# Optimization experiments

Hardware: AMD Instinct MI355X
Metric: run time of the kernel (lower is better)

## Reference

```python
import jax, jax.numpy as jnp
import numpy as np

E = 20    # number of residue types (rc.restypes)
NB = 2    # num_blocks per AngleHead
NA = 7    # num_angles
C_S = 384
C_H = 128
BS, L = 8, 2048


def setup_inputs() -> dict:
    key = jax.random.key(0)
    ks = jax.random.split(key, 16)
    sc = 0.02
    return {
        "s": jax.random.normal(ks[0], (BS, L, C_S), dtype=jnp.float32),
        "s_init": jax.random.normal(ks[1], (BS, L, C_S), dtype=jnp.float32),
        "aatype": jax.random.randint(ks[2], (BS, L), 0, E, dtype=jnp.int32),
        # stacked per-residue-type AngleHead params
        "Win": jax.random.normal(ks[3], (E, C_S, C_H), dtype=jnp.float32) * sc,
        "b_in": jax.random.normal(ks[4], (E, C_H), dtype=jnp.float32) * sc,
        "Winit": jax.random.normal(ks[5], (E, C_S, C_H), dtype=jnp.float32) * sc,
        "b_init2": jax.random.normal(ks[6], (E, C_H), dtype=jnp.float32) * sc,
        "Wb1": jax.random.normal(ks[7], (E, NB, C_H, C_H), dtype=jnp.float32) * sc,
        "bb1": jax.random.normal(ks[8], (E, NB, C_H), dtype=jnp.float32) * sc,
        "Wb2": jax.random.normal(ks[9], (E, NB, C_H, C_H), dtype=jnp.float32) * sc,
        "bb2": jax.random.normal(ks[10], (E, NB, C_H), dtype=jnp.float32) * sc,
        "Wout": jax.random.normal(ks[11], (E, C_H, NA * 2), dtype=jnp.float32) * sc,
        "b_out": jax.random.normal(ks[12], (E, NA * 2), dtype=jnp.float32) * sc,
    }


def reference(s, s_init, aatype, Win, b_in, Winit, b_init2, Wb1, bb1, Wb2, bb2, Wout, b_out):
    relu = jax.nn.relu
    bs, seq_len, c_s = s.shape
    N = bs * seq_len
    sf = s.reshape(N, c_s)          # [N, c_s]
    si = s_init.reshape(N, c_s)     # [N, c_s]

    # Dense dispatch: run every token through all E per-type heads, then
    # combine with the one-hot routing mask (math identical to the torch
    # gather/scatter loop over residue types).
    h = jnp.einsum('nd,edh->neh', relu(sf), Win) + b_in            # [N,E,H]
    h = h + jnp.einsum('nd,edh->neh', relu(si), Winit) + b_init2   # [N,E,H]

    for b in range(NB):  # ResidualBlock1d: s + W2 @ relu(W1 @ relu(s))
        a = jnp.einsum('neh,ehk->nek', relu(h), Wb1[:, b]) + bb1[:, b]
        a = jnp.einsum('nek,ekh->neh', relu(a), Wb2[:, b]) + bb2[:, b]
        h = h + a

    out = jnp.einsum('neh,eho->neo', relu(h), Wout) + b_out        # [N,E,2*NA]
    sel = jax.nn.one_hot(aatype.reshape(N), E, dtype=out.dtype)    # [N,E]
    ang = jnp.einsum('neo,ne->no', out, sel).reshape(bs, seq_len, NA, 2)

    # F.normalize(dim=-1): x / max(||x||, eps)
    nrm = jnp.maximum(jnp.linalg.norm(ang, axis=-1, keepdims=True), 1e-12)
    return ang / nrm
```

## Files before the change

### kernel.cpp

```cpp
#include <hip/hip_runtime.h>
#include <math.h>

#define E_TYPES 20
#define NBLK 2
#define NANG 7
#define CS 384
#define CH 128
#define N_TOK (8 * 2048)
#define TOK 32
#define TPB 256
#define KC 128
#define MAX_TILES (N_TOK / TOK + E_TYPES)
#define NPREP 64

#define HIST_OFF 0
#define CNT_OFF 1536
#define POFF_OFF 1600
#define PERM_OFF 2048

#define WT1_OFF (256 * 1024)
#define WT1_SZ  (20 * 8 * 24 * 2048)
#define WTR_OFF (WT1_OFF + WT1_SZ)

typedef __attribute__((ext_vector_type(8))) short bfrag;
typedef __attribute__((ext_vector_type(4))) float f32x4;

__device__ __forceinline__ void split_bf16(float x, unsigned short& h, unsigned short& l) {
    unsigned int u = __float_as_uint(x);
    unsigned int hb = (u + 0x7FFFu + ((u >> 16) & 1u)) & 0xFFFF0000u;
    h = (unsigned short)(hb >> 16);
    float r = x - __uint_as_float(hb);
    unsigned int v = __float_as_uint(r);
    l = (unsigned short)((v + 0x7FFFu + ((v >> 16) & 1u)) >> 16);
}

__global__ void prep1(const float* __restrict__ Win, const float* __restrict__ Winit,
                      const float* __restrict__ Wb1, const float* __restrict__ Wb2,
                      const int* __restrict__ aatype, int* __restrict__ wsI,
                      unsigned short* __restrict__ wt) {
    __shared__ int lh[E_TYPES];
    int bid = blockIdx.x;
    int t = threadIdx.x;
    if (bid >= 1600) {
        int b2 = bid - 1600;
        if (t < E_TYPES) lh[t] = 0;
        __syncthreads();
        int idx = b2 * 256 + t;
        if (idx < N_TOK) atomicAdd(&lh[aatype[idx]], 1);
        __syncthreads();
        if (t < E_TYPES) wsI[HIST_OFF + b2 * E_TYPES + t] = lh[t];
        return;
    }
    int gid = bid * 256 + t;
    unsigned short h[8], l[8];
    if (gid < 245760) {
        int lane = gid & 63;
        int bi = gid >> 6;
        int kb = bi % 24;
        int r = bi / 24;
        int nt = r & 7, e = r >> 3;
        int n = nt * 16 + (lane & 15);
        int k0 = kb * 32 + (lane >> 4) * 8;
        #pragma unroll
        for (int j = 0; j < 8; j++) {
            int k = k0 + j;
            float x = (k < CS) ? Win[((size_t)e * CS + k) * CH + n]
                               : Winit[((size_t)e * CS + (k - CS)) * CH + n];
            split_bf16(x, h[j], l[j]);
        }
        unsigned short* dst = wt + (WT1_OFF / 2) + (size_t)bi * 1024 + lane * 8;
        *(bfrag*)dst = *(bfrag*)h;
        *(bfrag*)(dst + 512) = *(bfrag*)l;
    } else {
        gid -= 245760;
        int lane = gid & 63;
        int bi = gid >> 6;
        int kb = bi & 3;
        int nt = (bi >> 2) & 7;
        int m4 = (bi >> 5) & 3;
        int e = bi >> 7;
        int b = m4 >> 1;
        const float* W = (m4 & 1) ? Wb2 : Wb1;
        int n = nt * 16 + (lane & 15);
        int k0 = kb * 32 + (lane >> 4) * 8;
        #pragma unroll
        for (int j = 0; j < 8; j++) {
            int k = k0 + j;
            float x = W[(((size_t)e * NBLK + b) * CH + k) * CH + n];
            split_bf16(x, h[j], l[j]);
        }
        unsigned short* dst = wt + (WTR_OFF / 2) + (size_t)bi * 1024 + lane * 8;
        *(bfrag*)dst = *(bfrag*)h;
        *(bfrag*)(dst + 512) = *(bfrag*)l;
    }
}

__global__ void scatter_k(const int* __restrict__ aatype, int* ws) {
    __shared__ int lhist[NPREP * E_TYPES];
    __shared__ int counts[E_TYPES], poff[E_TYPES + 1], mybase[E_TYPES], lcur[E_TYPES];
    int t = threadIdx.x;
    int bid = blockIdx.x;
    for (int idx = t; idx < NPREP * E_TYPES; idx += TPB)
        lhist[idx] = ws[HIST_OFF + idx];
    if (t < E_TYPES) lcur[t] = 0;
    __syncthreads();
    if (t < E_TYPES) {
        int tot = 0, pre = 0;
        for (int b = 0; b < NPREP; b++) {
            int v = lhist[b * E_TYPES + t];
            tot += v;
            if (b < bid) pre += v;
        }
        counts[t] = tot;
        mybase[t] = pre;
    }
    __syncthreads();
    if (t == 0) {
        int off = 0;
        for (int e = 0; e < E_TYPES; e++) {
            poff[e] = off;
            off += (counts[e] + TOK - 1) & ~(TOK - 1);
        }
        poff[E_TYPES] = off;
    }
    __syncthreads();
    if (t < E_TYPES) mybase[t] += poff[t];
    __syncthreads();
    int idx = bid * blockDim.x + t;
    if (idx < N_TOK) {
        int e = aatype[idx];
        int r = atomicAdd(&lcur[e], 1);
        ws[PERM_OFF + mybase[e] + r] = idx;
    }
    if (bid == 0) {
        if (t < E_TYPES) ws[CNT_OFF + t] = counts[t];
        if (t == 0)
            for (int e = 0; e <= E_TYPES; e++) ws[POFF_OFF + e] = poff[e];
    }
}

#define MFMA(a, b, c) __builtin_amdgcn_mfma_f32_16x16x32_bf16((a), (b), (c), 0, 0, 0)

__global__ __launch_bounds__(TPB)
void angle_main(const float* __restrict__ s, const float* __restrict__ si,
                const float* __restrict__ b_in, const float* __restrict__ b_init2,
                const float* __restrict__ bb1, const float* __restrict__ bb2,
                const float* __restrict__ Wout, const float* __restrict__ b_out,
                const int* __restrict__ wsI, const unsigned short* __restrict__ wt,
                float* __restrict__ out)
{
    __shared__ unsigned short Ah[TOK][136];
    __shared__ unsigned short Al[TOK][136];
    __shared__ float Hf[TOK][132];
    __shared__ float Of[TOK][16];
    __shared__ int ptok[TOK];

    int pos = blockIdx.x * TOK;
    if (pos >= wsI[POFF_OFF + E_TYPES]) return;
    int e = 0;
    while (e < E_TYPES - 1 && pos >= wsI[POFF_OFF + e + 1]) e++;
    int n = wsI[CNT_OFF + e] - (pos - wsI[POFF_OFF + e]);
    if (n > TOK) n = TOK;

    int t = threadIdx.x;
    if (t < TOK) ptok[t] = wsI[PERM_OFF + pos + ((t < n) ? t : 0)];

    int w = t >> 6, lane = t & 63;
    int lane15 = lane & 15, quad = lane >> 4;
    int nc[2] = { (2 * w) * 16 + lane15, (2 * w + 1) * 16 + lane15 };

    const bfrag* wt1 = (const bfrag*)((const char*)wt + WT1_OFF);
    const bfrag* wtr = (const bfrag*)((const char*)wt + WTR_OFF);

    f32x4 acc[2][2];
    {
        float bv0 = b_in[e * CH + nc[0]] + b_init2[e * CH + nc[0]];
        float bv1 = b_in[e * CH + nc[1]] + b_init2[e * CH + nc[1]];
        #pragma unroll
        for (int mt = 0; mt < 2; mt++) {
            acc[mt][0] = (f32x4){bv0, bv0, bv0, bv0};
            acc[mt][1] = (f32x4){bv1, bv1, bv1, bv1};
        }
    }

    __syncthreads();

    int srow = t >> 3;
    int scol = (t & 7) * 16;
    for (int c = 0; c < 6; c++) {
        const float* src = (c < 3) ? s : si;
        int kb0 = (c < 3 ? c : c - 3) * KC;
        {
            const float4* rp = (const float4*)(src + (size_t)ptok[srow] * CS + kb0 + scol);
            #pragma unroll
            for (int q = 0; q < 4; q++) {
                float4 v = rp[q];
                ushort4 hv, lv;
                split_bf16(fmaxf(v.x, 0.f), hv.x, lv.x);
                split_bf16(fmaxf(v.y, 0.f), hv.y, lv.y);
                split_bf16(fmaxf(v.z, 0.f), hv.z, lv.z);
                split_bf16(fmaxf(v.w, 0.f), hv.w, lv.w);
                *(ushort4*)&Ah[srow][scol + 4 * q] = hv;
                *(ushort4*)&Al[srow][scol + 4 * q] = lv;
            }
        }
        __syncthreads();
        #pragma unroll
        for (int ks = 0; ks < 4; ks++) {
            int kb = c * 4 + ks;
            int kl = ks * 32 + quad * 8;
            bfrag ah0 = *(const bfrag*)&Ah[lane15][kl];
            bfrag ah1 = *(const bfrag*)&Ah[16 + lane15][kl];
            bfrag al0 = *(const bfrag*)&Al[lane15][kl];
            bfrag al1 = *(const bfrag*)&Al[16 + lane15][kl];
            size_t b0 = ((size_t)(e * 8 + 2 * w) * 24 + kb) * 128;
            size_t b1 = ((size_t)(e * 8 + 2 * w + 1) * 24 + kb) * 128;
            bfrag bh0 = wt1[b0 + lane],      bl0 = wt1[b0 + 64 + lane];
            bfrag bh1 = wt1[b1 + lane],      bl1 = wt1[b1 + 64 + lane];
            acc[0][0] = MFMA(ah0, bh0, acc[0][0]);
            acc[0][0] = MFMA(ah0, bl0, acc[0][0]);
            acc[0][0] = MFMA(al0, bh0, acc[0][0]);
            acc[0][1] = MFMA(ah0, bh1, acc[0][1]);
            acc[0][1] = MFMA(ah0, bl1, acc[0][1]);
            acc[0][1] = MFMA(al0, bh1, acc[0][1]);
            acc[1][0] = MFMA(ah1, bh0, acc[1][0]);
            acc[1][0] = MFMA(ah1, bl0, acc[1][0]);
            acc[1][0] = MFMA(al1, bh0, acc[1][0]);
            acc[1][1] = MFMA(ah1, bh1, acc[1][1]);
            acc[1][1] = MFMA(ah1, bl1, acc[1][1]);
            acc[1][1] = MFMA(al1, bh1, acc[1][1]);
        }
        __syncthreads();
    }

    for (int b = 0; b < NBLK; b++) {
        #pragma unroll
        for (int mt = 0; mt < 2; mt++)
            #pragma unroll
            for (int nl = 0; nl < 2; nl++) {
                f32x4 v = acc[mt][nl];
                #pragma unroll
                for (int r = 0; r < 4; r++) {
                    int m = mt * 16 + quad * 4 + r;
                    unsigned short hh, ll;
                    split_bf16(fmaxf(v[r], 0.f), hh, ll);
                    Ah[m][nc[nl]] = hh;
                    Al[m][nc[nl]] = ll;
                }
            }
        __syncthreads();

        f32x4 a2[2][2];
        {
            float bv0 = bb1[(e * NBLK + b) * CH + nc[0]];
            float bv1 = bb1[(e * NBLK + b) * CH + nc[1]];
            #pragma unroll
            for (int mt = 0; mt < 2; mt++) {
                a2[mt][0] = (f32x4){bv0, bv0, bv0, bv0};
                a2[mt][1] = (f32x4){bv1, bv1, bv1, bv1};
            }
        }
        #pragma unroll
        for (int ks = 0; ks < 4; ks++) {
            int kl = ks * 32 + quad * 8;
            bfrag ah0 = *(const bfrag*)&Ah[lane15][kl];
            bfrag ah1 = *(const bfrag*)&Ah[16 + lane15][kl];
            bfrag al0 = *(const bfrag*)&Al[lane15][kl];
            bfrag al1 = *(const bfrag*)&Al[16 + lane15][kl];
            size_t b0 = (((size_t)(e * 4 + 2 * b) * 8 + 2 * w) * 4 + ks) * 128;
            size_t b1 = (((size_t)(e * 4 + 2 * b) * 8 + 2 * w + 1) * 4 + ks) * 128;
            bfrag bh0 = wtr[b0 + lane], bl0 = wtr[b0 + 64 + lane];
            bfrag bh1 = wtr[b1 + lane], bl1 = wtr[b1 + 64 + lane];
            a2[0][0] = MFMA(ah0, bh0, a2[0][0]);
            a2[0][0] = MFMA(ah0, bl0, a2[0][0]);
            a2[0][0] = MFMA(al0, bh0, a2[0][0]);
            a2[0][1] = MFMA(ah0, bh1, a2[0][1]);
            a2[0][1] = MFMA(ah0, bl1, a2[0][1]);
            a2[0][1] = MFMA(al0, bh1, a2[0][1]);
            a2[1][0] = MFMA(ah1, bh0, a2[1][0]);
            a2[1][0] = MFMA(ah1, bl0, a2[1][0]);
            a2[1][0] = MFMA(al1, bh0, a2[1][0]);
            a2[1][1] = MFMA(ah1, bh1, a2[1][1]);
            a2[1][1] = MFMA(ah1, bl1, a2[1][1]);
            a2[1][1] = MFMA(al1, bh1, a2[1][1]);
        }
        __syncthreads();

        #pragma unroll
        for (int mt = 0; mt < 2; mt++)
            #pragma unroll
            for (int nl = 0; nl < 2; nl++) {
                f32x4 v = a2[mt][nl];
                #pragma unroll
                for (int r = 0; r < 4; r++) {
                    int m = mt * 16 + quad * 4 + r;
                    unsigned short hh, ll;
                    split_bf16(fmaxf(v[r], 0.f), hh, ll);
                    Ah[m][nc[nl]] = hh;
                    Al[m][nc[nl]] = ll;
                }
            }
        __syncthreads();

        f32x4 a3[2][2];
        {
            float bv0 = bb2[(e * NBLK + b) * CH + nc[0]];
            float bv1 = bb2[(e * NBLK + b) * CH + nc[1]];
            #pragma unroll
            for (int mt = 0; mt < 2; mt++) {
                a3[mt][0] = (f32x4){bv0, bv0, bv0, bv0};
                a3[mt][1] = (f32x4){bv1, bv1, bv1, bv1};
            }
        }
        #pragma unroll
        for (int ks = 0; ks < 4; ks++) {
            int kl = ks * 32 + quad * 8;
            bfrag ah0 = *(const bfrag*)&Ah[lane15][kl];
            bfrag ah1 = *(const bfrag*)&Ah[16 + lane15][kl];
            bfrag al0 = *(const bfrag*)&Al[lane15][kl];
            bfrag al1 = *(const bfrag*)&Al[16 + lane15][kl];
            size_t b0 = (((size_t)(e * 4 + 2 * b + 1) * 8 + 2 * w) * 4 + ks) * 128;
            size_t b1 = (((size_t)(e * 4 + 2 * b + 1) * 8 + 2 * w + 1) * 4 + ks) * 128;
            bfrag bh0 = wtr[b0 + lane], bl0 = wtr[b0 + 64 + lane];
            bfrag bh1 = wtr[b1 + lane], bl1 = wtr[b1 + 64 + lane];
            a3[0][0] = MFMA(ah0, bh0, a3[0][0]);
            a3[0][0] = MFMA(ah0, bl0, a3[0][0]);
            a3[0][0] = MFMA(al0, bh0, a3[0][0]);
            a3[0][1] = MFMA(ah0, bh1, a3[0][1]);
            a3[0][1] = MFMA(ah0, bl1, a3[0][1]);
            a3[0][1] = MFMA(al0, bh1, a3[0][1]);
            a3[1][0] = MFMA(ah1, bh0, a3[1][0]);
            a3[1][0] = MFMA(ah1, bl0, a3[1][0]);
            a3[1][0] = MFMA(al1, bh0, a3[1][0]);
            a3[1][1] = MFMA(ah1, bh1, a3[1][1]);
            a3[1][1] = MFMA(ah1, bl1, a3[1][1]);
            a3[1][1] = MFMA(al1, bh1, a3[1][1]);
        }
        #pragma unroll
        for (int mt = 0; mt < 2; mt++)
            #pragma unroll
            for (int nl = 0; nl < 2; nl++)
                acc[mt][nl] += a3[mt][nl];
        __syncthreads();
    }

    #pragma unroll
    for (int mt = 0; mt < 2; mt++)
        #pragma unroll
        for (int nl = 0; nl < 2; nl++) {
            f32x4 v = acc[mt][nl];
            #pragma unroll
            for (int r = 0; r < 4; r++)
                Hf[mt * 16 + quad * 4 + r][nc[nl]] = fmaxf(v[r], 0.f);
        }
    __syncthreads();

    const float* WoutE = Wout + (size_t)e * CH * (NANG * 2);
    const float* boutE = b_out + (size_t)e * (NANG * 2);
    for (int idx = t; idx < n * (NANG * 2); idx += TPB) {
        int i = idx / (NANG * 2);
        int o = idx % (NANG * 2);
        float v = boutE[o];
        #pragma unroll 4
        for (int k = 0; k < CH; k++)
            v = fmaf(Hf[i][k], WoutE[(size_t)k * (NANG * 2) + o], v);
        Of[i][o] = v;
    }
    __syncthreads();

    for (int idx = t; idx < n * NANG; idx += TPB) {
        int i = idx / NANG;
        int a = idx % NANG;
        float x = Of[i][2 * a];
        float y = Of[i][2 * a + 1];
        float nr = fmaxf(sqrtf(x * x + y * y), 1e-12f);
        size_t base = (size_t)ptok[i] * (NANG * 2) + 2 * a;
        out[base]     = x / nr;
        out[base + 1] = y / nr;
    }
}

extern "C" void kernel_launch(void* const* d_in, const int* in_sizes, int n_in,
                              void* d_out, int out_size, void* d_ws, size_t ws_size,
                              hipStream_t stream) {
    const float* s       = (const float*)d_in[0];
    const float* s_init  = (const float*)d_in[1];
    const int*   aatype  = (const int*)d_in[2];
    const float* Win     = (const float*)d_in[3];
    const float* b_in    = (const float*)d_in[4];
    const float* Winit   = (const float*)d_in[5];
    const float* b_init2 = (const float*)d_in[6];
    const float* Wb1     = (const float*)d_in[7];
    const float* bb1     = (const float*)d_in[8];
    const float* Wb2     = (const float*)d_in[9];
    const float* bb2     = (const float*)d_in[10];
    const float* Wout    = (const float*)d_in[11];
    const float* b_out   = (const float*)d_in[12];
    int* wsI = (int*)d_ws;
    unsigned short* wt = (unsigned short*)d_ws;
    float* out = (float*)d_out;

    hipLaunchKernelGGL(prep1, dim3(1664), dim3(256), 0, stream,
                       Win, Winit, Wb1, Wb2, aatype, wsI, wt);
    hipLaunchKernelGGL(scatter_k, dim3(NPREP), dim3(TPB), 0, stream, aatype, wsI);
    hipLaunchKernelGGL(angle_main, dim3(MAX_TILES), dim3(TPB), 0, stream,
                       s, s_init, b_in, b_init2, bb1, bb2, Wout, b_out,
                       wsI, wt, out);
}
```

Before: 160.0 us.

## Use 512-thread blocks in main kernel with one column tile per wave and prefetch

```diff
diff --git a/kernel.cpp b/kernel.cpp
--- a/kernel.cpp
+++ b/kernel.cpp
@@ -9,6 +9,7 @@
 #define N_TOK (8 * 2048)
 #define TOK 32
 #define TPB 256
+#define TPB_MAIN 512
 #define KC 128
 #define MAX_TILES (N_TOK / TOK + E_TYPES)
 #define NPREP 64
@@ -141,7 +142,7 @@
 
 #define MFMA(a, b, c) __builtin_amdgcn_mfma_f32_16x16x32_bf16((a), (b), (c), 0, 0, 0)
 
-__global__ __launch_bounds__(TPB)
+__global__ __launch_bounds__(TPB_MAIN)
 void angle_main(const float* __restrict__ s, const float* __restrict__ si,
                 const float* __restrict__ b_in, const float* __restrict__ b_init2,
                 const float* __restrict__ bb1, const float* __restrict__ bb2,
@@ -167,44 +168,43 @@
 
     int w = t >> 6, lane = t & 63;
     int lane15 = lane & 15, quad = lane >> 4;
-    int nc[2] = { (2 * w) * 16 + lane15, (2 * w + 1) * 16 + lane15 };
+    int nc = w * 16 + lane15;
 
     const bfrag* wt1 = (const bfrag*)((const char*)wt + WT1_OFF);
     const bfrag* wtr = (const bfrag*)((const char*)wt + WTR_OFF);
 
-    f32x4 acc[2][2];
+    f32x4 acc[2];
     {
-        float bv0 = b_in[e * CH + nc[0]] + b_init2[e * CH + nc[0]];
-        float bv1 = b_in[e * CH + nc[1]] + b_init2[e * CH + nc[1]];
-        #pragma unroll
-        for (int mt = 0; mt < 2; mt++) {
-            acc[mt][0] = (f32x4){bv0, bv0, bv0, bv0};
-            acc[mt][1] = (f32x4){bv1, bv1, bv1, bv1};
-        }
-    }
-
-    __syncthreads();
-
-    int srow = t >> 3;
-    int scol = (t & 7) * 16;
+        float bv = b_in[e * CH + nc] + b_init2[e * CH + nc];
+        acc[0] = (f32x4){bv, bv, bv, bv};
+        acc[1] = acc[0];
+    }
+
+    __syncthreads();
+
+    int srow = t >> 4;
+    int scol = (t & 15) * 8;
+    size_t rowoff = (size_t)ptok[srow] * CS + scol;
+    float4 p0 = *(const float4*)(s + rowoff);
+    float4 p1 = *(const float4*)(s + rowoff + 4);
+
     for (int c = 0; c < 6; c++) {
-        const float* src = (c < 3) ? s : si;
-        int kb0 = (c < 3 ? c : c - 3) * KC;
         {
-            const float4* rp = (const float4*)(src + (size_t)ptok[srow] * CS + kb0 + scol);
+            float xv[8] = {p0.x, p0.y, p0.z, p0.w, p1.x, p1.y, p1.z, p1.w};
+            unsigned short h8[8], l8[8];
             #pragma unroll
-            for (int q = 0; q < 4; q++) {
-                float4 v = rp[q];
-                ushort4 hv, lv;
-                split_bf16(fmaxf(v.x, 0.f), hv.x, lv.x);
-                split_bf16(fmaxf(v.y, 0.f), hv.y, lv.y);
-                split_bf16(fmaxf(v.z, 0.f), hv.z, lv.z);
-                split_bf16(fmaxf(v.w, 0.f), hv.w, lv.w);
-                *(ushort4*)&Ah[srow][scol + 4 * q] = hv;
-                *(ushort4*)&Al[srow][scol + 4 * q] = lv;
-            }
-        }
-        __syncthreads();
+            for (int j = 0; j < 8; j++)
+                split_bf16(fmaxf(xv[j], 0.f), h8[j], l8[j]);
+            *(bfrag*)&Ah[srow][scol] = *(bfrag*)h8;
+            *(bfrag*)&Al[srow][scol] = *(bfrag*)l8;
+        }
+        __syncthreads();
+        if (c < 5) {
+            const float* src = (c + 1 < 3) ? s : si;
+            int kb0 = ((c + 1 < 3) ? (c + 1) : (c - 2)) * KC;
+            p0 = *(const float4*)(src + rowoff + kb0);
+            p1 = *(const float4*)(src + rowoff + kb0 + 4);
+        }
         #pragma unroll
         for (int ks = 0; ks < 4; ks++) {
             int kb = c * 4 + ks;
@@ -213,52 +213,39 @@
             bfrag ah1 = *(const bfrag*)&Ah[16 + lane15][kl];
             bfrag al0 = *(const bfrag*)&Al[lane15][kl];
             bfrag al1 = *(const bfrag*)&Al[16 + lane15][kl];
-            size_t b0 = ((size_t)(e * 8 + 2 * w) * 24 + kb) * 128;
-            size_t b1 = ((size_t)(e * 8 + 2 * w + 1) * 24 + kb) * 128;
-            bfrag bh0 = wt1[b0 + lane],      bl0 = wt1[b0 + 64 + lane];
-            bfrag bh1 = wt1[b1 + lane],      bl1 = wt1[b1 + 64 + lane];
-            acc[0][0] = MFMA(ah0, bh0, acc[0][0]);
-            acc[0][0] = MFMA(ah0, bl0, acc[0][0]);
-            acc[0][0] = MFMA(al0, bh0, acc[0][0]);
-            acc[0][1] = MFMA(ah0, bh1, acc[0][1]);
-            acc[0][1] = MFMA(ah0, bl1, acc[0][1]);
-            acc[0][1] = MFMA(al0, bh1, acc[0][1]);
-            acc[1][0] = MFMA(ah1, bh0, acc[1][0]);
-            acc[1][0] = MFMA(ah1, bl0, acc[1][0]);
-            acc[1][0] = MFMA(al1, bh0, acc[1][0]);
-            acc[1][1] = MFMA(ah1, bh1, acc[1][1]);
-            acc[1][1] = MFMA(ah1, bl1, acc[1][1]);
-            acc[1][1] = MFMA(al1, bh1, acc[1][1]);
+            size_t b0 = ((size_t)(e * 8 + w) * 24 + kb) * 128;
+            bfrag bh = wt1[b0 + lane];
+            bfrag bl = wt1[b0 + 64 + lane];
+            acc[0] = MFMA(ah0, bh, acc[0]);
+            acc[0] = MFMA(ah0, bl, acc[0]);
+            acc[0] = MFMA(al0, bh, acc[0]);
+            acc[1] = MFMA(ah1, bh, acc[1]);
+            acc[1] = MFMA(ah1, bl, acc[1]);
+            acc[1] = MFMA(al1, bh, acc[1]);
         }
         __syncthreads();
     }
 
     for (int b = 0; b < NBLK; b++) {
         #pragma unroll
-        for (int mt = 0; mt < 2; mt++)
+        for (int mt = 0; mt < 2; mt++) {
+            f32x4 v = acc[mt];
             #pragma unroll
-            for (int nl = 0; nl < 2; nl++) {
-                f32x4 v = acc[mt][nl];
-                #pragma unroll
-                for (int r = 0; r < 4; r++) {
-                    int m = mt * 16 + quad * 4 + r;
-                    unsigned short hh, ll;
-                    split_bf16(fmaxf(v[r], 0.f), hh, ll);
-                    Ah[m][nc[nl]] = hh;
-                    Al[m][nc[nl]] = ll;
-                }
+            for (int r = 0; r < 4; r++) {
+                int m = mt * 16 + quad * 4 + r;
+                unsigned short hh, ll;
+                split_bf16(fmaxf(v[r], 0.f), hh, ll);
+                Ah[m][nc] = hh;
+                Al[m][nc] = ll;
             }
-        __syncthreads();
-
-        f32x4 a2[2][2];
+        }
+        __syncthreads();
+
+        f32x4 a2[2];
         {
-            float bv0 = bb1[(e * NBLK + b) * CH + nc[0]];
-            float bv1 = bb1[(e * NBLK + b) * CH + nc[1]];
-            #pragma unroll
-            for (int mt = 0; mt < 2; mt++) {
-                a2[mt][0] = (f32x4){bv0, bv0, bv0, bv0};
-                a2[mt][1] = (f32x4){bv1, bv1, bv1, bv1};
-            }
+            float bv = bb1[(e * NBLK + b) * CH + nc];
+            a2[0] = (f32x4){bv, bv, bv, bv};
+            a2[1] = a2[0];
         }
         #pragma unroll
         for (int ks = 0; ks < 4; ks++) {
@@ -267,50 +254,36 @@
             bfrag ah1 = *(const bfrag*)&Ah[16 + lane15][kl];
             bfrag al0 = *(const bfrag*)&Al[lane15][kl];
             bfrag al1 = *(const bfrag*)&Al[16 + lane15][kl];
-            size_t b0 = (((size_t)(e * 4 + 2 * b) * 8 + 2 * w) * 4 + ks) * 128;
-            size_t b1 = (((size_t)(e * 4 + 2 * b) * 8 + 2 * w + 1) * 4 + ks) * 128;
-            bfrag bh0 = wtr[b0 + lane], bl0 = wtr[b0 + 64 + lane];
-            bfrag bh1 = wtr[b1 + lane], bl1 = wtr[b1 + 64 + lane];
-            a2[0][0] = MFMA(ah0, bh0, a2[0][0]);
-            a2[0][0] = MFMA(ah0, bl0, a2[0][0]);
-            a2[0][0] = MFMA(al0, bh0, a2[0][0]);
-            a2[0][1] = MFMA(ah0, bh1, a2[0][1]);
-            a2[0][1] = MFMA(ah0, bl1, a2[0][1]);
-            a2[0][1] = MFMA(al0, bh1, a2[0][1]);
-            a2[1][0] = MFMA(ah1, bh0, a2[1][0]);
-            a2[1][0] = MFMA(ah1, bl0, a2[1][0]);
-            a2[1][0] = MFMA(al1, bh0, a2[1][0]);
-            a2[1][1] = MFMA(ah1, bh1, a2[1][1]);
-            a2[1][1] = MFMA(ah1, bl1, a2[1][1]);
-            a2[1][1] = MFMA(al1, bh1, a2[1][1]);
-        }
-        __syncthreads();
-
-        #pragma unroll
-        for (int mt = 0; mt < 2; mt++)
+            size_t b0 = (((size_t)(e * 4 + 2 * b) * 8 + w) * 4 + ks) * 128;
+            bfrag bh = wtr[b0 + lane], bl = wtr[b0 + 64 + lane];
+            a2[0] = MFMA(ah0, bh, a2[0]);
+            a2[0] = MFMA(ah0, bl, a2[0]);
+            a2[0] = MFMA(al0, bh, a2[0]);
+            a2[1] = MFMA(ah1, bh, a2[1]);
+            a2[1] = MFMA(ah1, bl, a2[1]);
+            a2[1] = MFMA(al1, bh, a2[1]);
+        }
+        __syncthreads();
+
+        #pragma unroll
+        for (int mt = 0; mt < 2; mt++) {
+            f32x4 v = a2[mt];
             #pragma unroll
-            for (int nl = 0; nl < 2; nl++) {
-                f32x4 v = a2[mt][nl];
-                #pragma unroll
-                for (int r = 0; r < 4; r++) {
-                    int m = mt * 16 + quad * 4 + r;
-                    unsigned short hh, ll;
-                    split_bf16(fmaxf(v[r], 0.f), hh, ll);
-                    Ah[m][nc[nl]] = hh;
-                    Al[m][nc[nl]] = ll;
-                }
+            for (int r = 0; r < 4; r++) {
+                int m = mt * 16 + quad * 4 + r;
+                unsigned short hh, ll;
+                split_bf16(fmaxf(v[r], 0.f), hh, ll);
+                Ah[m][nc] = hh;
+                Al[m][nc] = ll;
             }
-        __syncthreads();
-
-        f32x4 a3[2][2];
+        }
+        __syncthreads();
+
+        f32x4 a3[2];
         {
-            float bv0 = bb2[(e * NBLK + b) * CH + nc[0]];
-            float bv1 = bb2[(e * NBLK + b) * CH + nc[1]];
-            #pragma unroll
-            for (int mt = 0; mt < 2; mt++) {
-                a3[mt][0] = (f32x4){bv0, bv0, bv0, bv0};
-                a3[mt][1] = (f32x4){bv1, bv1, bv1, bv1};
-            }
+            float bv = bb2[(e * NBLK + b) * CH + nc];
+            a3[0] = (f32x4){bv, bv, bv, bv};
+            a3[1] = a3[0];
         }
         #pragma unroll
         for (int ks = 0; ks < 4; ks++) {
@@ -319,58 +292,49 @@
             bfrag ah1 = *(const bfrag*)&Ah[16 + lane15][kl];
             bfrag al0 = *(const bfrag*)&Al[lane15][kl];
             bfrag al1 = *(const bfrag*)&Al[16 + lane15][kl];
-            size_t b0 = (((size_t)(e * 4 + 2 * b + 1) * 8 + 2 * w) * 4 + ks) * 128;
-            size_t b1 = (((size_t)(e * 4 + 2 * b + 1) * 8 + 2 * w + 1) * 4 + ks) * 128;
-            bfrag bh0 = wtr[b0 + lane], bl0 = wtr[b0 + 64 + lane];
-            bfrag bh1 = wtr[b1 + lane], bl1 = wtr[b1 + 64 + lane];
-            a3[0][0] = MFMA(ah0, bh0, a3[0][0]);
-            a3[0][0] = MFMA(ah0, bl0, a3[0][0]);
-            a3[0][0] = MFMA(al0, bh0, a3[0][0]);
-            a3[0][1] = MFMA(ah0, bh1, a3[0][1]);
-            a3[0][1] = MFMA(ah0, bl1, a3[0][1]);
-            a3[0][1] = MFMA(al0, bh1, a3[0][1]);
-            a3[1][0] = MFMA(ah1, bh0, a3[1][0]);
-            a3[1][0] = MFMA(ah1, bl0, a3[1][0]);
-            a3[1][0] = MFMA(al1, bh0, a3[1][0]);
-            a3[1][1] = MFMA(ah1, bh1, a3[1][1]);
-            a3[1][1] = MFMA(ah1, bl1, a3[1][1]);
-            a3[1][1] = MFMA(al1, bh1, a3[1][1]);
-        }
-        #pragma unroll
-        for (int mt = 0; mt < 2; mt++)
-            #pragma unroll
-            for (int nl = 0; nl < 2; nl++)
-                acc[mt][nl] += a3[mt][nl];
+            size_t b0 = (((size_t)(e * 4 + 2 * b + 1) * 8 + w) * 4 + ks) * 128;
+            bfrag bh = wtr[b0 + lane], bl = wtr[b0 + 64 + lane];
+            a3[0] = MFMA(ah0, bh, a3[0]);
+            a3[0] = MFMA(ah0, bl, a3[0]);
+            a3[0] = MFMA(al0, bh, a3[0]);
+            a3[1] = MFMA(ah1, bh, a3[1]);
+            a3[1] = MFMA(ah1, bl, a3[1]);
+            a3[1] = MFMA(al1, bh, a3[1]);
+        }
+        acc[0] += a3[0];
+        acc[1] += a3[1];
         __syncthreads();
     }
 
     #pragma unroll
-    for (int mt = 0; mt < 2; mt++)
-        #pragma unroll
-        for (int nl = 0; nl < 2; nl++) {
-            f32x4 v = acc[mt][nl];
-            #pragma unroll
-            for (int r = 0; r < 4; r++)
-                Hf[mt * 16 + quad * 4 + r][nc[nl]] = fmaxf(v[r], 0.f);
-        }
+    for (int mt = 0; mt < 2; mt++) {
+        f32x4 v = acc[mt];
+        #pragma unroll
+        for (int r = 0; r < 4; r++)
+            Hf[mt * 16 + quad * 4 + r][nc] = fmaxf(v[r], 0.f);
+    }
     __syncthreads();
 
     const float* WoutE = Wout + (size_t)e * CH * (NANG * 2);
     const float* boutE = b_out + (size_t)e * (NANG * 2);
-    for (int idx = t; idx < n * (NANG * 2); idx += TPB) {
+    for (int idx = t; idx < n * (NANG * 2); idx += TPB_MAIN) {
         int i = idx / (NANG * 2);
-        int o = idx % (NANG * 2);
-        float v = boutE[o];
+        int o = idx - i * (NANG * 2);
+        float v0 = boutE[o], v1 = 0.f, v2 = 0.f, v3 = 0.f;
         #pragma unroll 4
-        for (int k = 0; k < CH; k++)
-            v = fmaf(Hf[i][k], WoutE[(size_t)k * (NANG * 2) + o], v);
-        Of[i][o] = v;
-    }
-    __syncthreads();
-
-    for (int idx = t; idx < n * NANG; idx += TPB) {
+        for (int k = 0; k < CH; k += 4) {
+            v0 = fmaf(Hf[i][k],     WoutE[(size_t)k * (NANG * 2) + o],       v0);
+            v1 = fmaf(Hf[i][k + 1], WoutE[(size_t)(k + 1) * (NANG * 2) + o], v1);
+            v2 = fmaf(Hf[i][k + 2], WoutE[(size_t)(k + 2) * (NANG * 2) + o], v2);
+            v3 = fmaf(Hf[i][k + 3], WoutE[(size_t)(k + 3) * (NANG * 2) + o], v3);
+        }
+        Of[i][o] = (v0 + v1) + (v2 + v3);
+    }
+    __syncthreads();
+
+    for (int idx = t; idx < n * NANG; idx += TPB_MAIN) {
         int i = idx / NANG;
-        int a = idx % NANG;
+        int a = idx - i * NANG;
         float x = Of[i][2 * a];
         float y = Of[i][2 * a + 1];
         float nr = fmaxf(sqrtf(x * x + y * y), 1e-12f);
@@ -403,7 +367,7 @@
     hipLaunchKernelGGL(prep1, dim3(1664), dim3(256), 0, stream,
                        Win, Winit, Wb1, Wb2, aatype, wsI, wt);
     hipLaunchKernelGGL(scatter_k, dim3(NPREP), dim3(TPB), 0, stream, aatype, wsI);
-    hipLaunchKernelGGL(angle_main, dim3(MAX_TILES), dim3(TPB), 0, stream,
+    hipLaunchKernelGGL(angle_main, dim3(MAX_TILES), dim3(TPB_MAIN), 0, stream,
                        s, s_init, b_in, b_init2, bb1, bb2, Wout, b_out,
                        wsI, wt, out);
 }
```

Result: no change. 160.0 us (+0.0%).
